# Performance work log

Hardware: AMD Instinct MI355X
Metric: run time of the kernel (lower is better)

Reference implementation:

```python
import jax, jax.numpy as jnp
import numpy as np

H = 1024
N_HEADS = 16
DK = H // N_HEADS
B = 4
S_TGT = 1024
S_SRC = 1024
LN_EPS = 1e-5


def _ln(x, g, b):
    m = jnp.mean(x, axis=-1, keepdims=True)
    v = jnp.mean(jnp.square(x - m), axis=-1, keepdims=True)
    return (x - m) * jax.lax.rsqrt(v + LN_EPS) * g + b


def _mha(q_in, k_in, v_in, wq, wk, wv, wo, mask):
    # Equivalent to torch split(hidden//n_splits)+cat(dim=0) head layout:
    # per-(batch,head) scaled dot-product attention.
    Bq, Sq, _ = q_in.shape
    Sk = k_in.shape[1]
    q = (q_in @ wq).reshape(Bq, Sq, N_HEADS, DK)
    k = (k_in @ wk).reshape(Bq, Sk, N_HEADS, DK)
    v = (v_in @ wv).reshape(Bq, Sk, N_HEADS, DK)
    scores = jnp.einsum('bqhd,bkhd->bhqk', q, k)
    if mask is not None:
        scores = jnp.where(mask[:, None, :, :], -jnp.inf, scores)
    attn = jax.nn.softmax(scores / np.sqrt(DK).astype(np.float32), axis=-1)
    ctx = jnp.einsum('bhqk,bkhd->bqhd', attn, v).reshape(Bq, Sq, H)
    return ctx @ wo


def setup_inputs() -> dict:
    key = jax.random.key(0)
    ks = jax.random.split(key, 16)
    std = 1.0 / np.sqrt(H)
    p = {
        'x': jax.random.normal(ks[0], (B, S_TGT, H), jnp.float32),
        'key_and_value': jax.random.normal(ks[1], (B, S_SRC, H), jnp.float32),
        'mask': jnp.zeros((B, S_TGT, S_SRC), jnp.bool_),  # no padding
        # causal mask: True above the diagonal (masked positions)
        'future_mask': jnp.broadcast_to(
            jnp.triu(jnp.ones((S_TGT, S_TGT), jnp.bool_), k=1), (B, S_TGT, S_TGT)),
        'sa_wq': jax.random.normal(ks[2], (H, H), jnp.float32) * std,
        'sa_wk': jax.random.normal(ks[3], (H, H), jnp.float32) * std,
        'sa_wv': jax.random.normal(ks[4], (H, H), jnp.float32) * std,
        'sa_wo': jax.random.normal(ks[5], (H, H), jnp.float32) * std,
        'ca_wq': jax.random.normal(ks[6], (H, H), jnp.float32) * std,
        'ca_wk': jax.random.normal(ks[7], (H, H), jnp.float32) * std,
        'ca_wv': jax.random.normal(ks[8], (H, H), jnp.float32) * std,
        'ca_wo': jax.random.normal(ks[9], (H, H), jnp.float32) * std,
        'fc_w1': jax.random.normal(ks[10], (H, 4 * H), jnp.float32) * std,
        'fc_b1': jnp.zeros((4 * H,), jnp.float32),
        'fc_w2': jax.random.normal(ks[11], (4 * H, H), jnp.float32) * (0.5 * std),
        'fc_b2': jnp.zeros((H,), jnp.float32),
        'ln1_g': jnp.ones((H,), jnp.float32), 'ln1_b': jnp.zeros((H,), jnp.float32),
        'ln2_g': jnp.ones((H,), jnp.float32), 'ln2_b': jnp.zeros((H,), jnp.float32),
        'ln3_g': jnp.ones((H,), jnp.float32), 'ln3_b': jnp.zeros((H,), jnp.float32),
    }
    return p


def reference(x, key_and_value, mask, future_mask,
              sa_wq, sa_wk, sa_wv, sa_wo,
              ca_wq, ca_wk, ca_wv, ca_wo,
              fc_w1, fc_b1, fc_w2, fc_b2,
              ln1_g, ln1_b, ln2_g, ln2_b, ln3_g, ln3_b):
    # prev is None path (training); dropout in eval mode = identity.
    z = _ln(x, ln1_g, ln1_b)
    z = x + _mha(z, z, z, sa_wq, sa_wk, sa_wv, sa_wo, future_mask)
    nkv = _ln(key_and_value, ln2_g, ln2_b)
    z = z + _mha(_ln(z, ln2_g, ln2_b), nkv, nkv, ca_wq, ca_wk, ca_wv, ca_wo, mask)
    h = jax.nn.relu(_ln(z, ln3_g, ln3_b) @ fc_w1 + fc_b1)
    z = z + (h @ fc_w2 + fc_b2)
    return z
```

## Files before the change

### kernel.cpp

```cpp
#include <hip/hip_runtime.h>
#include <hip/hip_bf16.h>

typedef __attribute__((ext_vector_type(8))) short short8;
typedef __attribute__((ext_vector_type(4))) float f32x4;
using bf16 = __hip_bfloat16;

__device__ __forceinline__ void gload16(const void* g, void* l) {
  __builtin_amdgcn_global_load_lds(
      (const __attribute__((address_space(1))) void*)g,
      (__attribute__((address_space(3))) void*)l, 16, 0, 0);
}

__device__ __forceinline__ short f2bf(float f) {
  bf16 h = __float2bfloat16(f);
  short s;
  __builtin_memcpy(&s, &h, 2);
  return s;
}

__global__ __launch_bounds__(256)
void wtr8(const float* w0, const float* w1, const float* w2, const float* w3,
          const float* w4, const float* w5, const float* w6, const float* w7,
          bf16* __restrict__ Wout) {
  __shared__ float tile[32][33];
  const float* w;
  switch (blockIdx.z) {
    case 0: w = w0; break; case 1: w = w1; break;
    case 2: w = w2; break; case 3: w = w3; break;
    case 4: w = w4; break; case 5: w = w5; break;
    case 6: w = w6; break; default: w = w7; break;
  }
  bf16* wt = Wout + (size_t)blockIdx.z * 1024 * 1024;
  const int tx = threadIdx.x & 31, ty = threadIdx.x >> 5;
  const int c0 = blockIdx.x * 32, r0 = blockIdx.y * 32;
#pragma unroll
  for (int i = 0; i < 4; ++i)
    tile[ty * 4 + i][tx] = w[(size_t)(r0 + ty * 4 + i) * 1024 + c0 + tx];
  __syncthreads();
#pragma unroll
  for (int i = 0; i < 4; ++i) {
    const int cc = ty * 4 + i;
    wt[(size_t)(c0 + cc) * 1024 + r0 + tx] = __float2bfloat16(tile[tx][cc]);
  }
}

__global__ __launch_bounds__(256)
void wtr(const float* __restrict__ w, bf16* __restrict__ wt, int R, int C) {
  __shared__ float tile[32][33];
  const int tx = threadIdx.x & 31, ty = threadIdx.x >> 5;
  const int c0 = blockIdx.x * 32, r0 = blockIdx.y * 32;
#pragma unroll
  for (int i = 0; i < 4; ++i)
    tile[ty * 4 + i][tx] = w[(size_t)(r0 + ty * 4 + i) * C + c0 + tx];
  __syncthreads();
#pragma unroll
  for (int i = 0; i < 4; ++i) {
    const int cc = ty * 4 + i;
    wt[(size_t)(c0 + cc) * R + r0 + tx] = __float2bfloat16(tile[tx][cc]);
  }
}

__global__ __launch_bounds__(256)
void ln_k(const float* __restrict__ x, const float* __restrict__ g,
          const float* __restrict__ b, bf16* __restrict__ y) {
  const int row = blockIdx.x, t = threadIdx.x;
  const int wv = t >> 6, l = t & 63;
  const float4 v = reinterpret_cast<const float4*>(x + (size_t)row * 1024)[t];
  float s = v.x + v.y + v.z + v.w;
  float s2 = v.x * v.x + v.y * v.y + v.z * v.z + v.w * v.w;
#pragma unroll
  for (int m = 1; m < 64; m <<= 1) {
    s += __shfl_xor(s, m, 64);
    s2 += __shfl_xor(s2, m, 64);
  }
  __shared__ float ps[4], ps2[4];
  if (l == 0) { ps[wv] = s; ps2[wv] = s2; }
  __syncthreads();
  s = ps[0] + ps[1] + ps[2] + ps[3];
  s2 = ps2[0] + ps2[1] + ps2[2] + ps2[3];
  const float mean = s * (1.f / 1024.f);
  const float var = s2 * (1.f / 1024.f) - mean * mean;
  const float rs = rsqrtf(var + 1e-5f);
  const float4 gg = reinterpret_cast<const float4*>(g)[t];
  const float4 bb = reinterpret_cast<const float4*>(b)[t];
  ushort4 o;
  o.x = (unsigned short)f2bf((v.x - mean) * rs * gg.x + bb.x);
  o.y = (unsigned short)f2bf((v.y - mean) * rs * gg.y + bb.y);
  o.z = (unsigned short)f2bf((v.z - mean) * rs * gg.z + bb.z);
  o.w = (unsigned short)f2bf((v.w - mean) * rs * gg.w + bb.w);
  reinterpret_cast<ushort4*>(y + (size_t)row * 1024)[t] = o;
}

template <int BM, int EPI>
__global__ __launch_bounds__(256, 2)
void gemm_bt(const bf16* __restrict__ A, const bf16* __restrict__ BT,
             const float* bias, const float* res, void* outp,
             int M, int N, int K, bf16* vtp, int nv0) {
  constexpr int WM = BM / 32;
  constexpr int APASS = BM / 32;
  __shared__ alignas(16) short al[2][BM * 64];
  __shared__ alignas(16) short bl[2][128 * 64];
  const int t = threadIdx.x;
  const int gx = N >> 7;
  const int nwg = gridDim.x * gridDim.y;
  int id = blockIdx.y * gridDim.x + blockIdx.x;
  id = (id & 7) * (nwg >> 3) + (id >> 3);
  const int bx = id % gx, by = id / gx;
  const int m0 = by * BM, n0 = bx * 128;
  const int wv = t >> 6, l = t & 63, lr = l & 15, lk = l >> 4;
  const int wr = wv >> 1, wc = wv & 1;
  const int tr = t >> 3, tc = (t & 7) * 8;
  const int tcs = (((t & 7) ^ (tr & 7)) * 8);
  const int cro0 = ((lk ^ (lr & 7)) * 8);
  const int cro1 = (((4 + lk) ^ (lr & 7)) * 8);

  f32x4 acc[WM][4];
#pragma unroll
  for (int i = 0; i < WM; ++i)
#pragma unroll
    for (int j = 0; j < 4; ++j) acc[i][j] = (f32x4)0.f;

#define STAGE(buf, k0)                                                        \
  do {                                                                        \
    _Pragma("unroll") for (int it = 0; it < APASS; ++it) {                    \
      const int row = it * 32 + tr;                                           \
      gload16(A + (size_t)(m0 + row) * K + (k0) + tcs,                        \
              (char*)&al[buf][row * 64 + tc]);                                \
    }                                                                         \
    _Pragma("unroll") for (int it = 0; it < 4; ++it) {                        \
      const int row = it * 32 + tr;                                           \
      gload16(BT + (size_t)(n0 + row) * K + (k0) + tcs,                       \
              (char*)&bl[buf][row * 64 + tc]);                                \
    }                                                                         \
  } while (0)

#define COMPUTE(cur)                                                          \
  do {                                                                        \
    _Pragma("unroll") for (int ks = 0; ks < 2; ++ks) {                        \
      const int cro = ks ? cro1 : cro0;                                       \
      short8 af[WM], bfv[4];                                                  \
      _Pragma("unroll") for (int m = 0; m < WM; ++m) af[m] =                  \
          *reinterpret_cast<const short8*>(                                   \
              &al[cur][(wr * (BM / 2) + m * 16 + lr) * 64 + cro]);            \
      _Pragma("unroll") for (int n = 0; n < 4; ++n) bfv[n] =                  \
          *reinterpret_cast<const short8*>(                                   \
              &bl[cur][(wc * 64 + n * 16 + lr) * 64 + cro]);                  \
      _Pragma("unroll") for (int m = 0; m < WM; ++m)                          \
          _Pragma("unroll") for (int n = 0; n < 4; ++n) acc[m][n] =           \
              __builtin_amdgcn_mfma_f32_16x16x32_bf16(af[m], bfv[n],          \
                                                      acc[m][n], 0, 0, 0);    \
    }                                                                         \
  } while (0)

  const int nt = K >> 6;
  if constexpr (BM == 64) {
    STAGE(0, 0);
    STAGE(1, 64);
    for (int tk = 0; tk < nt; ++tk) {
      const int cur = tk & 1;
      if (tk < nt - 1)
        asm volatile("s_waitcnt vmcnt(6)" ::: "memory");
      else
        asm volatile("s_waitcnt vmcnt(0)" ::: "memory");
      __builtin_amdgcn_s_barrier();
      COMPUTE(cur);
      if (tk + 2 < nt) {
        asm volatile("s_waitcnt lgkmcnt(0)" ::: "memory");
        __builtin_amdgcn_s_barrier();
        STAGE(cur, (tk + 2) << 6);
      }
    }
  } else {
    STAGE(0, 0);
    asm volatile("s_waitcnt vmcnt(0)" ::: "memory");
    __syncthreads();
    for (int tk = 0; tk < nt; ++tk) {
      const int cur = tk & 1;
      if (tk + 1 < nt) STAGE(cur ^ 1, (tk + 1) << 6);
      COMPUTE(cur);
      asm volatile("s_waitcnt vmcnt(0)" ::: "memory");
      __syncthreads();
    }
  }
#undef STAGE
#undef COMPUTE

  const int r0 = m0 + wr * (BM / 2), c0 = n0 + wc * 64;
  if constexpr (EPI == 4) {
#pragma unroll
    for (int m = 0; m < WM; ++m) {
      const int rowb = r0 + m * 16 + lk * 4;
      const int bb = rowb >> 10, s0 = rowb & 1023;
#pragma unroll
      for (int n = 0; n < 4; ++n) {
        const int col = c0 + n * 16 + lr;
        if (col < nv0) {
#pragma unroll
          for (int r = 0; r < 4; ++r)
            ((bf16*)outp)[(size_t)(rowb + r) * nv0 + col] =
                __float2bfloat16(acc[m][n][r]);
        } else {
          ushort4 u;
          u.x = (unsigned short)f2bf(acc[m][n][0]);
          u.y = (unsigned short)f2bf(acc[m][n][1]);
          u.z = (unsigned short)f2bf(acc[m][n][2]);
          u.w = (unsigned short)f2bf(acc[m][n][3]);
          const size_t vidx = ((size_t)bb * 1024 + (col - nv0)) * 1024 + s0;
          *reinterpret_cast<ushort4*>(vtp + vidx) = u;
        }
      }
    }
  } else {
#pragma unroll
    for (int m = 0; m < WM; ++m)
#pragma unroll
      for (int n = 0; n < 4; ++n) {
        const int col = c0 + n * 16 + lr;
#pragma unroll
        for (int r = 0; r < 4; ++r) {
          const int row = r0 + m * 16 + lk * 4 + r;
          const size_t idx = (size_t)row * N + col;
          float v = acc[m][n][r];
          if (EPI == 0) {
            ((bf16*)outp)[idx] = __float2bfloat16(v);
          } else if (EPI == 1) {
            ((float*)outp)[idx] = res[idx] + v;
          } else if (EPI == 2) {
            v += bias[col];
            ((bf16*)outp)[idx] = __float2bfloat16(fmaxf(v, 0.f));
          } else {
            ((float*)outp)[idx] = res[idx] + v + bias[col];
          }
        }
      }
  }
}

__global__ __launch_bounds__(512, 1)
void gemm256(const bf16* __restrict__ A, const bf16* __restrict__ BT,
             const float* __restrict__ bias, bf16* __restrict__ outp,
             int M, int N, int K) {
  __shared__ alignas(16) short al[2][256 * 64];
  __shared__ alignas(16) short bl[2][256 * 64];
  const int t = threadIdx.x;
  const int gx = N >> 8;
  const int nwg = gridDim.x * gridDim.y;
  int id = blockIdx.y * gridDim.x + blockIdx.x;
  id = (id & 7) * (nwg >> 3) + (id >> 3);
  const int bx = id % gx, by = id / gx;
  const int m0 = by * 256, n0 = bx * 256;
  const int wid = t >> 6, l = t & 63, lr = l & 15, lk = l >> 4;
  const int wm = wid >> 2, wn = wid & 3;
  const int tr = t >> 3, tc = (t & 7) * 8;
  const int tcs = (((t & 7) ^ (tr & 7)) * 8);
  const int cro0 = ((lk ^ (lr & 7)) * 8);
  const int cro1 = (((4 + lk) ^ (lr & 7)) * 8);

  f32x4 acc[8][4];
#pragma unroll
  for (int i = 0; i < 8; ++i)
#pragma unroll
    for (int j = 0; j < 4; ++j) acc[i][j] = (f32x4)0.f;

#define STAGE2(buf, k0)                                                       \
  do {                                                                        \
    _Pragma("unroll") for (int it = 0; it < 4; ++it) {                        \
      const int row = it * 64 + tr;                                           \
      gload16(A + (size_t)(m0 + row) * K + (k0) + tcs,                        \
              (char*)&al[buf][row * 64 + tc]);                                \
    }                                                                         \
    _Pragma("unroll") for (int it = 0; it < 4; ++it) {                        \
      const int row = it * 64 + tr;                                           \
      gload16(BT + (size_t)(n0 + row) * K + (k0) + tcs,                       \
              (char*)&bl[buf][row * 64 + tc]);                                \
    }                                                                         \
  } while (0)

#define COMPUTE2(cur)                                                         \
  do {                                                                        \
    _Pragma("unroll") for (int ks = 0; ks < 2; ++ks) {                        \
      const int cro = ks ? cro1 : cro0;                                       \
      short8 af[8], bfv[4];                                                   \
      _Pragma("unroll") for (int m = 0; m < 8; ++m) af[m] =                   \
          *reinterpret_cast<const short8*>(                                   \
              &al[cur][(wm * 128 + m * 16 + lr) * 64 + cro]);                 \
      _Pragma("unroll") for (int n = 0; n < 4; ++n) bfv[n] =                  \
          *reinterpret_cast<const short8*>(                                   \
              &bl[cur][(wn * 64 + n * 16 + lr) * 64 + cro]);                  \
      _Pragma("unroll") for (int m = 0; m < 8; ++m)                           \
          _Pragma("unroll") for (int n = 0; n < 4; ++n) acc[m][n] =           \
              __builtin_amdgcn_mfma_f32_16x16x32_bf16(af[m], bfv[n],          \
                                                      acc[m][n], 0, 0, 0);    \
    }                                                                         \
  } while (0)

  const int nt = K >> 6;
  STAGE2(0, 0);
  STAGE2(1, 64);
  for (int tk = 0; tk < nt; ++tk) {
    const int cur = tk & 1;
    if (tk < nt - 1)
      asm volatile("s_waitcnt vmcnt(8)" ::: "memory");
    else
      asm volatile("s_waitcnt vmcnt(0)" ::: "memory");
    __builtin_amdgcn_s_barrier();
    COMPUTE2(cur);
    if (tk + 2 < nt) {
      asm volatile("s_waitcnt lgkmcnt(0)" ::: "memory");
      __builtin_amdgcn_s_barrier();
      STAGE2(cur, (tk + 2) << 6);
    }
  }

  const int r0 = m0 + wm * 128, c0 = n0 + wn * 64;
#pragma unroll
  for (int m = 0; m < 8; ++m)
#pragma unroll
    for (int n = 0; n < 4; ++n) {
      const int col = c0 + n * 16 + lr;
      const float bcol = bias[col];
#pragma unroll
      for (int r = 0; r < 4; ++r) {
        const int row = r0 + m * 16 + lk * 4 + r;
        const float v = acc[m][n][r] + bcol;
        outp[(size_t)row * N + col] = __float2bfloat16(fmaxf(v, 0.f));
      }
    }
#undef STAGE2
#undef COMPUTE2
}

__global__ __launch_bounds__(512, 1)
void gemm256_dual(const bf16* __restrict__ A0, const bf16* __restrict__ BT0,
                  bf16* __restrict__ out0, bf16* __restrict__ vt0,
                  const bf16* __restrict__ A1, const bf16* __restrict__ BT1,
                  bf16* __restrict__ out1, bf16* __restrict__ vt1) {
  __shared__ alignas(16) short al[2][256 * 64];
  __shared__ alignas(16) short bl[2][256 * 64];
  const int t = threadIdx.x;
  const int raw = blockIdx.x;
  const int id = (raw & 7) * 40 + (raw >> 3);
  const bf16 *A, *BT;
  bf16 *outp, *vtp;
  int nv0, gx, pid;
  if (id < 192) {
    A = A0; BT = BT0; outp = out0; vtp = vt0; nv0 = 2048; gx = 12; pid = id;
  } else {
    A = A1; BT = BT1; outp = out1; vtp = vt1; nv0 = 1024; gx = 8;
    pid = id - 192;
  }
  const int K = 1024;
  const int bx = pid % gx, by = pid / gx;
  const int m0 = by * 256, n0 = bx * 256;
  const int wid = t >> 6, l = t & 63, lr = l & 15, lk = l >> 4;
  const int wm = wid >> 2, wn = wid & 3;
  const int tr = t >> 3, tc = (t & 7) * 8;
  const int tcs = (((t & 7) ^ (tr & 7)) * 8);
  const int cro0 = ((lk ^ (lr & 7)) * 8);
  const int cro1 = (((4 + lk) ^ (lr & 7)) * 8);

  f32x4 acc[8][4];
#pragma unroll
  for (int i = 0; i < 8; ++i)
#pragma unroll
    for (int j = 0; j < 4; ++j) acc[i][j] = (f32x4)0.f;

#define STAGE2(buf, k0)                                                       \
  do {                                                                        \
    _Pragma("unroll") for (int it = 0; it < 4; ++it) {                        \
      const int row = it * 64 + tr;                                           \
      gload16(A + (size_t)(m0 + row) * K + (k0) + tcs,                        \
              (char*)&al[buf][row * 64 + tc]);                                \
    }                                                                         \
    _Pragma("unroll") for (int it = 0; it < 4; ++it) {                        \
      const int row = it * 64 + tr;                                           \
      gload16(BT + (size_t)(n0 + row) * K + (k0) + tcs,                       \
              (char*)&bl[buf][row * 64 + tc]);                                \
    }                                                                         \
  } while (0)

#define COMPUTE2(cur)                                                         \
  do {                                                                        \
    _Pragma("unroll") for (int ks = 0; ks < 2; ++ks) {                        \
      const int cro = ks ? cro1 : cro0;                                       \
      short8 af[8], bfv[4];                                                   \
      _Pragma("unroll") for (int m = 0; m < 8; ++m) af[m] =                   \
          *reinterpret_cast<const short8*>(                                   \
              &al[cur][(wm * 128 + m * 16 + lr) * 64 + cro]);                 \
      _Pragma("unroll") for (int n = 0; n < 4; ++n) bfv[n] =                  \
          *reinterpret_cast<const short8*>(                                   \
              &bl[cur][(wn * 64 + n * 16 + lr) * 64 + cro]);                  \
      _Pragma("unroll") for (int m = 0; m < 8; ++m)                           \
          _Pragma("unroll") for (int n = 0; n < 4; ++n) acc[m][n] =           \
              __builtin_amdgcn_mfma_f32_16x16x32_bf16(af[m], bfv[n],          \
                                                      acc[m][n], 0, 0, 0);    \
    }                                                                         \
  } while (0)

  const int nt = K >> 6;
  STAGE2(0, 0);
  STAGE2(1, 64);
  for (int tk = 0; tk < nt; ++tk) {
    const int cur = tk & 1;
    if (tk < nt - 1)
      asm volatile("s_waitcnt vmcnt(8)" ::: "memory");
    else
      asm volatile("s_waitcnt vmcnt(0)" ::: "memory");
    __builtin_amdgcn_s_barrier();
    COMPUTE2(cur);
    if (tk + 2 < nt) {
      asm volatile("s_waitcnt lgkmcnt(0)" ::: "memory");
      __builtin_amdgcn_s_barrier();
      STAGE2(cur, (tk + 2) << 6);
    }
  }
#undef STAGE2
#undef COMPUTE2

  const int r0 = m0 + wm * 128, c0 = n0 + wn * 64;
#pragma unroll
  for (int m = 0; m < 8; ++m) {
    const int rowb = r0 + m * 16 + lk * 4;
    const int bb = rowb >> 10, s0 = rowb & 1023;
#pragma unroll
    for (int n = 0; n < 4; ++n) {
      const int col = c0 + n * 16 + lr;
      if (col < nv0) {
#pragma unroll
        for (int r = 0; r < 4; ++r)
          outp[(size_t)(rowb + r) * nv0 + col] =
              __float2bfloat16(acc[m][n][r]);
      } else {
        ushort4 u;
        u.x = (unsigned short)f2bf(acc[m][n][0]);
        u.y = (unsigned short)f2bf(acc[m][n][1]);
        u.z = (unsigned short)f2bf(acc[m][n][2]);
        u.w = (unsigned short)f2bf(acc[m][n][3]);
        const size_t vidx = ((size_t)bb * 1024 + (col - nv0)) * 1024 + s0;
        *reinterpret_cast<ushort4*>(vtp + vidx) = u;
      }
    }
  }
}

template <bool CAUSAL>
__global__ __launch_bounds__(256, 2)
void flash8(const bf16* __restrict__ Qb, int ldq,
            const bf16* __restrict__ Kb, int ldk,
            const bf16* __restrict__ VTb, bf16* __restrict__ Ob) {
  __shared__ alignas(16) short kl[3][64 * 64];
  __shared__ alignas(16) short vl[3][64 * 64];
  __shared__ alignas(16) short pl[4][32 * 72];
  const int t = threadIdx.x, wv = t >> 6, l = t & 63, lr = l & 15, lk = l >> 4;
  const int raw = blockIdx.y * 8 + blockIdx.x;
  const int id = (raw & 7) * 64 + (raw >> 3);
  const int qb = id & 7, bh = id >> 3;
  const int b = bh >> 4, h = bh & 15;
  const size_t rowbase = (size_t)b * 1024;
  const int q0 = qb * 128 + wv * 32;
  const bf16* Vbase = VTb + (rowbase + h * 64) * 1024;

  const int tr = t >> 3;
  const int tcd = (t & 7) * 8;
  const int tcs = (((t & 7) ^ (tr & 7)) * 8);
  const int cro0 = ((lk ^ (lr & 7)) * 8);
  const int cro1 = (((4 + lk) ^ (lr & 7)) * 8);

  short8 qf[2][2];
#pragma unroll
  for (int m = 0; m < 2; ++m)
#pragma unroll
    for (int ks = 0; ks < 2; ++ks)
      qf[m][ks] = *reinterpret_cast<const short8*>(
          Qb + (rowbase + q0 + m * 16 + lr) * ldq + h * 64 + ks * 32 + lk * 8);

  short8 ones;
#pragma unroll
  for (int j = 0; j < 8; ++j) ones[j] = (short)0x3F80;

  f32x4 accO[2][4];
  f32x4 accL[2];
#pragma unroll
  for (int m = 0; m < 2; ++m) {
#pragma unroll
    for (int n = 0; n < 4; ++n) accO[m][n] = (f32x4)0.f;
    accL[m] = (f32x4)0.f;
  }

  const int ntb = CAUSAL ? (qb * 2 + 2) : 16;
  const int myLast = q0 >> 6;

#define FSTAGE(buf, kv0)                                                      \
  do {                                                                        \
    _Pragma("unroll") for (int it = 0; it < 2; ++it) {                        \
      const int row = it * 32 + tr;                                           \
      gload16(Kb + (rowbase + (kv0) + row) * ldk + h * 64 + tcs,              \
              (char*)&kl[buf][row * 64 + tcd]);                               \
    }                                                                         \
    _Pragma("unroll") for (int it = 0; it < 2; ++it) {                        \
      const int row = it * 32 + tr;                                           \
      gload16(Vbase + (size_t)row * 1024 + (kv0) + tcs,                       \
              (char*)&vl[buf][row * 64 + tcd]);                               \
    }                                                                         \
  } while (0)

  FSTAGE(0, 0);
  FSTAGE(1, 64);
  int cur = 0;
  for (int tk = 0; tk < ntb; ++tk) {
    if (tk < ntb - 1)
      asm volatile("s_waitcnt vmcnt(4)" ::: "memory");
    else
      asm volatile("s_waitcnt vmcnt(0)" ::: "memory");
    __builtin_amdgcn_s_barrier();
    if (tk + 2 < ntb) {
      int stg = cur + 2;
      if (stg >= 3) stg -= 3;
      FSTAGE(stg, (tk + 2) << 6);
    }
    if (!CAUSAL || tk <= myLast) {
      const int kv0 = tk * 64;
      const bool needmask = CAUSAL && (tk == myLast);
      f32x4 sa[2][4];
#pragma unroll
      for (int m = 0; m < 2; ++m)
#pragma unroll
        for (int n = 0; n < 4; ++n) sa[m][n] = (f32x4)0.f;
#pragma unroll
      for (int ks = 0; ks < 2; ++ks) {
        const int cro = ks ? cro1 : cro0;
        short8 kf[4];
#pragma unroll
        for (int n = 0; n < 4; ++n)
          kf[n] = *reinterpret_cast<const short8*>(
              &kl[cur][(n * 16 + lr) * 64 + cro]);
        __builtin_amdgcn_s_setprio(1);
#pragma unroll
        for (int m = 0; m < 2; ++m)
#pragma unroll
          for (int n = 0; n < 4; ++n)
            sa[m][n] = __builtin_amdgcn_mfma_f32_16x16x32_bf16(
                qf[m][ks], kf[n], sa[m][n], 0, 0, 0);
        __builtin_amdgcn_s_setprio(0);
      }
#pragma unroll
      for (int m = 0; m < 2; ++m) {
#pragma unroll
        for (int r = 0; r < 4; ++r) {
          const int row = q0 + m * 16 + lk * 4 + r;
          float s0 = sa[m][0][r] * 0.125f, s1 = sa[m][1][r] * 0.125f;
          float s2 = sa[m][2][r] * 0.125f, s3 = sa[m][3][r] * 0.125f;
          if (needmask) {
            if (kv0 + 0 + lr > row) s0 = -1e30f;
            if (kv0 + 16 + lr > row) s1 = -1e30f;
            if (kv0 + 32 + lr > row) s2 = -1e30f;
            if (kv0 + 48 + lr > row) s3 = -1e30f;
          }
          const float p0 = __expf(s0), p1 = __expf(s1);
          const float p2 = __expf(s2), p3 = __expf(s3);
          const int prow = m * 16 + lk * 4 + r;
          pl[wv][prow * 72 + lr + 0] = f2bf(p0);
          pl[wv][prow * 72 + lr + 16] = f2bf(p1);
          pl[wv][prow * 72 + lr + 32] = f2bf(p2);
          pl[wv][prow * 72 + lr + 48] = f2bf(p3);
        }
      }
#pragma unroll
      for (int ks = 0; ks < 2; ++ks) {
        const int cro = ks ? cro1 : cro0;
        short8 pf[2], vf[4];
#pragma unroll
        for (int m = 0; m < 2; ++m)
          pf[m] = *reinterpret_cast<const short8*>(
              &pl[wv][(m * 16 + lr) * 72 + ks * 32 + lk * 8]);
#pragma unroll
        for (int n = 0; n < 4; ++n)
          vf[n] = *reinterpret_cast<const short8*>(
              &vl[cur][(n * 16 + lr) * 64 + cro]);
        __builtin_amdgcn_s_setprio(1);
#pragma unroll
        for (int m = 0; m < 2; ++m) {
#pragma unroll
          for (int n = 0; n < 4; ++n)
            accO[m][n] = __builtin_amdgcn_mfma_f32_16x16x32_bf16(
                pf[m], vf[n], accO[m][n], 0, 0, 0);
          accL[m] = __builtin_amdgcn_mfma_f32_16x16x32_bf16(
              pf[m], ones, accL[m], 0, 0, 0);
        }
        __builtin_amdgcn_s_setprio(0);
      }
    }
    cur = (cur + 1 == 3) ? 0 : cur + 1;
  }
#undef FSTAGE

#pragma unroll
  for (int m = 0; m < 2; ++m)
#pragma unroll
    for (int n = 0; n < 4; ++n)
#pragma unroll
      for (int r = 0; r < 4; ++r) {
        const int row = q0 + m * 16 + lk * 4 + r;
        const int col = n * 16 + lr;
        const float o = accO[m][n][r] / accL[m][r];
        Ob[(rowbase + row) * 1024 + h * 64 + col] = __float2bfloat16(o);
      }
}

extern "C" void kernel_launch(void* const* d_in, const int* in_sizes, int n_in,
                              void* d_out, int out_size, void* d_ws,
                              size_t ws_size, hipStream_t stream) {
  const float* x = (const float*)d_in[0];
  const float* kv_in = (const float*)d_in[1];
  const float* sa_wq = (const float*)d_in[4];
  const float* sa_wk = (const float*)d_in[5];
  const float* sa_wv = (const float*)d_in[6];
  const float* sa_wo = (const float*)d_in[7];
  const float* ca_wq = (const float*)d_in[8];
  const float* ca_wk = (const float*)d_in[9];
  const float* ca_wv = (const float*)d_in[10];
  const float* ca_wo = (const float*)d_in[11];
  const float* fc_w1 = (const float*)d_in[12];
  const float* fc_b1 = (const float*)d_in[13];
  const float* fc_w2 = (const float*)d_in[14];
  const float* fc_b2 = (const float*)d_in[15];
  const float* ln1_g = (const float*)d_in[16];
  const float* ln1_b = (const float*)d_in[17];
  const float* ln2_g = (const float*)d_in[18];
  const float* ln2_b = (const float*)d_in[19];
  const float* ln3_g = (const float*)d_in[20];
  const float* ln3_b = (const float*)d_in[21];

  char* ws = (char*)d_ws;
  const size_t MB = 1024 * 1024;
  bf16* W = (bf16*)ws;
  bf16* w1T = W + 8 * MB;
  bf16* w2T = W + 12 * MB;
  float* z = (float*)(ws + 32 * MB);
  bf16* t0 = (bf16*)(ws + 48 * MB);
  bf16* qkvb = (bf16*)(ws + 56 * MB);
  bf16* vts = (bf16*)(ws + 72 * MB);
  bf16* kb = (bf16*)(ws + 80 * MB);
  bf16* vtc = (bf16*)(ws + 88 * MB);
  bf16* qb = (bf16*)(ws + 96 * MB);
  bf16* ctx = (bf16*)(ws + 104 * MB);
  bf16* kvln = (bf16*)(ws + 112 * MB);
  bf16* hb = (bf16*)(ws + 120 * MB);

  const dim3 B256(256);
  wtr8<<<dim3(32, 32, 8), B256, 0, stream>>>(sa_wq, sa_wk, sa_wv, sa_wo,
                                             ca_wq, ca_wk, ca_wv, ca_wo, W);
  wtr<<<dim3(128, 32), B256, 0, stream>>>(fc_w1, w1T, 1024, 4096);
  wtr<<<dim3(32, 128), B256, 0, stream>>>(fc_w2, w2T, 4096, 1024);

  ln_k<<<4096, B256, 0, stream>>>(x, ln1_g, ln1_b, t0);
  ln_k<<<4096, B256, 0, stream>>>(kv_in, ln2_g, ln2_b, kvln);
  gemm256_dual<<<dim3(320), dim3(512), 0, stream>>>(
      t0, W, qkvb, vts, kvln, W + 5 * MB, kb, vtc);

  flash8<true><<<dim3(8, 64), B256, 0, stream>>>(
      qkvb, 2048, qkvb + 1024, 2048, vts, ctx);
  gemm_bt<64, 1><<<dim3(8, 64), B256, 0, stream>>>(
      ctx, W + 3 * MB, nullptr, x, z, 4096, 1024, 1024, nullptr, 0);

  ln_k<<<4096, B256, 0, stream>>>(z, ln2_g, ln2_b, t0);
  gemm_bt<64, 0><<<dim3(8, 64), B256, 0, stream>>>(
      t0, W + 4 * MB, nullptr, nullptr, qb, 4096, 1024, 1024, nullptr, 0);
  flash8<false><<<dim3(8, 64), B256, 0, stream>>>(
      qb, 1024, kb, 1024, vtc, ctx);
  gemm_bt<64, 1><<<dim3(8, 64), B256, 0, stream>>>(
      ctx, W + 7 * MB, nullptr, z, z, 4096, 1024, 1024, nullptr, 0);

  ln_k<<<4096, B256, 0, stream>>>(z, ln3_g, ln3_b, t0);
  gemm256<<<dim3(16, 16), dim3(512), 0, stream>>>(
      t0, w1T, fc_b1, hb, 4096, 4096, 1024);
  gemm_bt<64, 3><<<dim3(8, 64), B256, 0, stream>>>(
      hb, w2T, fc_b2, z, d_out, 4096, 1024, 4096, nullptr, 0);
}
```

Baseline: 333.2 us.

## Split-K the FFN down-projection with 256-tile GEMM and a bf16 partial reduce

The FFN second GEMM (K=4096) moves from the 64x128 tile kernel to the 256x256 kernel, split four ways along K through blockIdx.z. Each split writes a bf16 partial into the workspace. A new elementwise kernel sums the four partials and adds the residual and bias in fp32. The aim is more work per tile and enough workgroups to fill the GPU, at the cost of an extra kernel launch, extra memory traffic for the partials, and extra rounding from storing them in bf16.

```diff
diff --git a/kernel.cpp b/kernel.cpp
--- a/kernel.cpp
+++ b/kernel.cpp
@@ -16,6 +16,13 @@
   short s;
   __builtin_memcpy(&s, &h, 2);
   return s;
+}
+
+__device__ __forceinline__ float bf2f(unsigned short u) {
+  unsigned int x = ((unsigned int)u) << 16;
+  float f;
+  __builtin_memcpy(&f, &x, 4);
+  return f;
 }
 
 __global__ __launch_bounds__(256)
@@ -89,6 +96,23 @@
   o.z = (unsigned short)f2bf((v.z - mean) * rs * gg.z + bb.z);
   o.w = (unsigned short)f2bf((v.w - mean) * rs * gg.w + bb.w);
   reinterpret_cast<ushort4*>(y + (size_t)row * 1024)[t] = o;
+}
+
+__global__ __launch_bounds__(256)
+void ffn_add4b(const ushort4* __restrict__ p0, const ushort4* __restrict__ p1,
+               const ushort4* __restrict__ p2, const ushort4* __restrict__ p3,
+               const float4* __restrict__ res, const float4* __restrict__ bias,
+               float4* __restrict__ out) {
+  const size_t i = (size_t)blockIdx.x * 256 + threadIdx.x;
+  const ushort4 a = p0[i], b = p1[i], c = p2[i], d = p3[i];
+  const float4 r = res[i];
+  const float4 g = bias[i & 255];
+  float4 o;
+  o.x = (bf2f(a.x) + bf2f(b.x)) + (bf2f(c.x) + bf2f(d.x)) + r.x + g.x;
+  o.y = (bf2f(a.y) + bf2f(b.y)) + (bf2f(c.y) + bf2f(d.y)) + r.y + g.y;
+  o.z = (bf2f(a.z) + bf2f(b.z)) + (bf2f(c.z) + bf2f(d.z)) + r.z + g.z;
+  o.w = (bf2f(a.w) + bf2f(b.w)) + (bf2f(c.w) + bf2f(d.w)) + r.w + g.w;
+  out[i] = o;
 }
 
 template <int BM, int EPI>
@@ -236,10 +260,11 @@
   }
 }
 
+template <int EPI>
 __global__ __launch_bounds__(512, 1)
 void gemm256(const bf16* __restrict__ A, const bf16* __restrict__ BT,
-             const float* __restrict__ bias, bf16* __restrict__ outp,
-             int M, int N, int K) {
+             const float* __restrict__ bias, void* __restrict__ outp,
+             int M, int N, int K, int lda) {
   __shared__ alignas(16) short al[2][256 * 64];
   __shared__ alignas(16) short bl[2][256 * 64];
   const int t = threadIdx.x;
@@ -256,6 +281,9 @@
   const int cro0 = ((lk ^ (lr & 7)) * 8);
   const int cro1 = (((4 + lk) ^ (lr & 7)) * 8);
 
+  const bf16* Ab = (EPI == 5) ? A + (size_t)blockIdx.z * K : A;
+  const bf16* BTb = (EPI == 5) ? BT + (size_t)blockIdx.z * K : BT;
+
   f32x4 acc[8][4];
 #pragma unroll
   for (int i = 0; i < 8; ++i)
@@ -266,12 +294,12 @@
   do {                                                                        \
     _Pragma("unroll") for (int it = 0; it < 4; ++it) {                        \
       const int row = it * 64 + tr;                                           \
-      gload16(A + (size_t)(m0 + row) * K + (k0) + tcs,                        \
+      gload16(Ab + (size_t)(m0 + row) * lda + (k0) + tcs,                     \
               (char*)&al[buf][row * 64 + tc]);                                \
     }                                                                         \
     _Pragma("unroll") for (int it = 0; it < 4; ++it) {                        \
       const int row = it * 64 + tr;                                           \
-      gload16(BT + (size_t)(n0 + row) * K + (k0) + tcs,                       \
+      gload16(BTb + (size_t)(n0 + row) * lda + (k0) + tcs,                    \
               (char*)&bl[buf][row * 64 + tc]);                                \
     }                                                                         \
   } while (0)
@@ -311,23 +339,39 @@
       STAGE2(cur, (tk + 2) << 6);
     }
   }
-
-  const int r0 = m0 + wm * 128, c0 = n0 + wn * 64;
-#pragma unroll
-  for (int m = 0; m < 8; ++m)
-#pragma unroll
-    for (int n = 0; n < 4; ++n) {
-      const int col = c0 + n * 16 + lr;
-      const float bcol = bias[col];
-#pragma unroll
-      for (int r = 0; r < 4; ++r) {
-        const int row = r0 + m * 16 + lk * 4 + r;
-        const float v = acc[m][n][r] + bcol;
-        outp[(size_t)row * N + col] = __float2bfloat16(fmaxf(v, 0.f));
-      }
-    }
 #undef STAGE2
 #undef COMPUTE2
+
+  const int r0 = m0 + wm * 128, c0 = n0 + wn * 64;
+  if constexpr (EPI == 2) {
+#pragma unroll
+    for (int m = 0; m < 8; ++m)
+#pragma unroll
+      for (int n = 0; n < 4; ++n) {
+        const int col = c0 + n * 16 + lr;
+        const float bcol = bias[col];
+#pragma unroll
+        for (int r = 0; r < 4; ++r) {
+          const int row = r0 + m * 16 + lk * 4 + r;
+          const float v = acc[m][n][r] + bcol;
+          ((bf16*)outp)[(size_t)row * N + col] =
+              __float2bfloat16(fmaxf(v, 0.f));
+        }
+      }
+  } else {
+    bf16* po = (bf16*)outp + (size_t)blockIdx.z * M * N;
+#pragma unroll
+    for (int m = 0; m < 8; ++m)
+#pragma unroll
+      for (int n = 0; n < 4; ++n) {
+        const int col = c0 + n * 16 + lr;
+#pragma unroll
+        for (int r = 0; r < 4; ++r) {
+          const int row = r0 + m * 16 + lk * 4 + r;
+          po[(size_t)row * N + col] = __float2bfloat16(acc[m][n][r]);
+        }
+      }
+  }
 }
 
 __global__ __launch_bounds__(512, 1)
@@ -646,6 +690,7 @@
   bf16* ctx = (bf16*)(ws + 104 * MB);
   bf16* kvln = (bf16*)(ws + 112 * MB);
   bf16* hb = (bf16*)(ws + 120 * MB);
+  bf16* partsb = (bf16*)(ws + 56 * MB);
 
   const dim3 B256(256);
   wtr8<<<dim3(32, 32, 8), B256, 0, stream>>>(sa_wq, sa_wk, sa_wv, sa_wo,
@@ -672,8 +717,14 @@
       ctx, W + 7 * MB, nullptr, z, z, 4096, 1024, 1024, nullptr, 0);
 
   ln_k<<<4096, B256, 0, stream>>>(z, ln3_g, ln3_b, t0);
-  gemm256<<<dim3(16, 16), dim3(512), 0, stream>>>(
-      t0, w1T, fc_b1, hb, 4096, 4096, 1024);
-  gemm_bt<64, 3><<<dim3(8, 64), B256, 0, stream>>>(
-      hb, w2T, fc_b2, z, d_out, 4096, 1024, 4096, nullptr, 0);
-}
+  gemm256<2><<<dim3(16, 16), dim3(512), 0, stream>>>(
+      t0, w1T, fc_b1, hb, 4096, 4096, 1024, 1024);
+  gemm256<5><<<dim3(4, 16, 4), dim3(512), 0, stream>>>(
+      hb, w2T, nullptr, partsb, 4096, 1024, 1024, 4096);
+  ffn_add4b<<<4096, B256, 0, stream>>>(
+      (const ushort4*)(partsb + 0 * (size_t)4096 * 1024),
+      (const ushort4*)(partsb + 1 * (size_t)4096 * 1024),
+      (const ushort4*)(partsb + 2 * (size_t)4096 * 1024),
+      (const ushort4*)(partsb + 3 * (size_t)4096 * 1024),
+      (const float4*)z, (const float4*)fc_b2, (float4*)d_out);
+}
```

Result: no change. 328.3 us (-1.5%).
